# Kernel tuning notes

Hardware: AMD Instinct MI355X
Metric: run time of the kernel (lower is better)

Reference implementation:

```python
import jax, jax.numpy as jnp
import numpy as np

N = 100000      # nodes
E = 800000      # edges (avg degree 8)
F = 61          # num_node_features (embedding dim); node feat = F+3 = 64 with pos
D = 64          # hidden_dim
OUT = 32        # output_dim
TYPES = 100     # num_node_types
G = 64          # number of graphs in the batch (global_mean_pool segments)
L = 4           # num_layers per SE3Transformer (from transformer_config)


def _mk(k, shape):
    return jax.random.normal(k, shape, jnp.float32) * 0.1


def setup_inputs() -> dict:
    key = jax.random.key(0)
    ks = jax.random.split(key, 24)
    din = F + 3  # cat([pos, embedding(z)])
    inp = {
        "pos": jax.random.normal(ks[0], (N, 3), jnp.float32),
        "z": jax.random.randint(ks[1], (N,), 0, TYPES),
        "edge_index": jax.random.randint(ks[2], (2, E), 0, N),
        "batch": jnp.sort(jax.random.randint(ks[3], (N,), 0, G)),
        "emb": _mk(ks[4], (TYPES, F)),
        # transformer1: input proj din->D, then L message-passing layers at width D
        "t1_Win": _mk(ks[5], (din, D)),
        "t1_W1": _mk(ks[6], (L, 2 * D + 1, D)), "t1_b1": jnp.zeros((L, D), jnp.float32),
        "t1_W2": _mk(ks[7], (L, D, D)),        "t1_b2": jnp.zeros((L, D), jnp.float32),
        "t1_W3": _mk(ks[8], (L, 2 * D, D)),    "t1_b3": jnp.zeros((L, D), jnp.float32),
        # transformer2: input proj D->D, then L layers at width D
        "t2_Win": _mk(ks[9], (D, D)),
        "t2_W1": _mk(ks[10], (L, 2 * D + 1, D)), "t2_b1": jnp.zeros((L, D), jnp.float32),
        "t2_W2": _mk(ks[11], (L, D, D)),         "t2_b2": jnp.zeros((L, D), jnp.float32),
        "t2_W3": _mk(ks[12], (L, 2 * D, D)),     "t2_b3": jnp.zeros((L, D), jnp.float32),
        # final Linear(hidden_dim, output_dim)
        "Wlin": _mk(ks[13], (D, OUT)), "blin": jnp.zeros((OUT,), jnp.float32),
    }
    return inp


def _transformer(h, pos, src, dst, Win, W1, b1, W2, b2, W3, b3):
    """Equivariant graph transformer block: input projection + L distance-
    conditioned message-passing layers with residual updates."""
    h = h @ Win  # [N, D]
    # squared pairwise distance per edge -> rotation/translation invariant
    d2 = jnp.sum((pos[src] - pos[dst]) ** 2, axis=-1, keepdims=True)  # [E, 1]

    def layer(h, p):
        W1, b1, W2, b2, W3, b3 = p
        m = jnp.concatenate([h[src], h[dst], d2], axis=-1)        # [E, 2D+1]
        m = jax.nn.relu(m @ W1 + b1) @ W2 + b2                    # [E, D]
        agg = jax.ops.segment_sum(m, dst, num_segments=N)          # [N, D]
        h = h + jax.nn.relu(jnp.concatenate([h, agg], axis=-1) @ W3 + b3)
        return h, None

    h, _ = jax.lax.scan(layer, h, (W1, b1, W2, b2, W3, b3))
    return h


def reference(pos, z, edge_index, batch, emb,
              t1_Win, t1_W1, t1_b1, t1_W2, t1_b2, t1_W3, t1_b3,
              t2_Win, t2_W1, t2_b1, t2_W2, t2_b2, t2_W3, t2_b3,
              Wlin, blin):
    src, dst = edge_index[0], edge_index[1]
    x = jnp.concatenate([pos, emb[z]], axis=-1)  # [N, 3+F]
    x = jax.nn.relu(_transformer(x, pos, src, dst, t1_Win, t1_W1, t1_b1, t1_W2, t1_b2, t1_W3, t1_b3))
    x = jax.nn.relu(_transformer(x, pos, src, dst, t2_Win, t2_W1, t2_b1, t2_W2, t2_b2, t2_W3, t2_b3))
    x = x @ Wlin + blin  # [N, OUT]
    # global_mean_pool over graph ids
    counts = jax.ops.segment_sum(jnp.ones((N,), x.dtype), batch, num_segments=G)
    pooled = jax.ops.segment_sum(x, batch, num_segments=G) / jnp.clip(counts, 1.0)[:, None]
    return pooled  # [G, OUT]
```

## Files before the change

### kernel.cpp

```cpp
#include <hip/hip_runtime.h>
#include <hip/hip_bf16.h>

typedef unsigned short u16;
typedef unsigned int   u32;
typedef short bf16x8 __attribute__((ext_vector_type(8)));
typedef float f32x4  __attribute__((ext_vector_type(4)));
typedef int   i32x2  __attribute__((ext_vector_type(2)));

#define NN 100000
#define EE 800000
#define NTILE 6250
#define NTB   1563
#define EBLK  1536
#define TOTW  (EBLK * 4)
#define SCB   98
#define GMAX  (NN + EE / 8 + 2)

#define MFMA16(a,b,c) __builtin_amdgcn_mfma_f32_16x16x32_bf16(a,b,c,0,0,0)

__device__ __forceinline__ float b2f(u16 u) {
    u32 x = ((u32)u) << 16;
    return __uint_as_float(x);
}
__device__ __forceinline__ u16 f2b(float f) {
    __hip_bfloat16 h = __float2bfloat16(f);
    return *reinterpret_cast<u16*>(&h);
}
__device__ __forceinline__ void splt(float v, u16& hi, u16& lo) {
    hi = f2b(v);
    lo = f2b(v - b2f(hi));
}

__global__ __launch_bounds__(256) void k_deg(const int* __restrict__ dst,
                                             int* __restrict__ deg) {
    int e = blockIdx.x * 256 + threadIdx.x;
    if (e < EE) atomicAdd(&deg[dst[e]], 1);
}

__global__ __launch_bounds__(1024) void k_scanA(const int* __restrict__ deg,
                                                int* __restrict__ part) {
    __shared__ int s[1024];
    int i = blockIdx.x * 1024 + threadIdx.x;
    int v = (i < NN) ? deg[i] : 0;
    s[threadIdx.x] = v;
    __syncthreads();
    for (int off = 512; off > 0; off >>= 1) {
        if ((int)threadIdx.x < off) s[threadIdx.x] += s[threadIdx.x + off];
        __syncthreads();
    }
    if (threadIdx.x == 0) part[blockIdx.x] = s[0];
}

__global__ void k_scanB(int* __restrict__ part) {
    if (threadIdx.x == 0 && blockIdx.x == 0) {
        int run = 0;
        for (int b = 0; b < SCB; ++b) { int v = part[b]; part[b] = run; run += v; }
        part[SCB] = run;
    }
}

__global__ __launch_bounds__(1024) void k_scanC(const int* __restrict__ deg,
                                                const int* __restrict__ part,
                                                int* __restrict__ rowptr) {
    __shared__ int s[1024];
    int i = blockIdx.x * 1024 + threadIdx.x;
    int v = (i < NN) ? deg[i] : 0;
    s[threadIdx.x] = v;
    __syncthreads();
    for (int off = 1; off < 1024; off <<= 1) {
        int t = ((int)threadIdx.x >= off) ? s[threadIdx.x - off] : 0;
        __syncthreads();
        s[threadIdx.x] += t;
        __syncthreads();
    }
    int incl = s[threadIdx.x];
    if (i < NN) rowptr[i] = part[blockIdx.x] + incl - v;
    if (i == NN - 1) rowptr[NN] = part[SCB];
}

__global__ __launch_bounds__(256) void k_scatter(const int* __restrict__ src,
                                                 const int* __restrict__ dst,
                                                 const float* __restrict__ pos,
                                                 const int* __restrict__ rowptr,
                                                 const int* __restrict__ grp_ptr,
                                                 int* __restrict__ cursor,
                                                 int* __restrict__ srcg,
                                                 float* __restrict__ d2g) {
    int e = blockIdx.x * 256 + threadIdx.x;
    if (e >= EE) return;
    int d = dst[e], s = src[e];
    int p = atomicAdd(&cursor[d], 1);
    int off = p - rowptr[d];
    long slot = (long)(grp_ptr[d] + (off >> 3)) * 8 + (off & 7);
    srcg[slot] = s;
    float dx = pos[s * 3 + 0] - pos[d * 3 + 0];
    float dy = pos[s * 3 + 1] - pos[d * 3 + 1];
    float dz = pos[s * 3 + 2] - pos[d * 3 + 2];
    d2g[slot] = dx * dx + dy * dy + dz * dz;
}

__global__ __launch_bounds__(256) void k_ngrp(const int* __restrict__ deg,
                                              int* __restrict__ ngrp) {
    int i = blockIdx.x * 256 + threadIdx.x;
    if (i < NN) ngrp[i] = (deg[i] + 7) >> 3;
}

__global__ __launch_bounds__(256) void k_gtab(const int* __restrict__ deg,
                                              const int* __restrict__ grp_ptr,
                                              int* __restrict__ gtab) {
    int n = blockIdx.x * 256 + threadIdx.x;
    if (n >= NN) return;
    int d = deg[n];
    int ng = (d + 7) >> 3;
    int base = grp_ptr[n];
    for (int k = 0; k < ng; ++k) {
        int cc = d - 8 * k; if (cc > 8) cc = 8;
        gtab[base + k] = (n << 4) | cc;
    }
}

__global__ __launch_bounds__(256) void k_swz(const float* t1W1, const float* t1W2, const float* t1W3,
                                             const float* t2W1, const float* t2W2, const float* t2W3,
                                             const float* t1Win, const float* t2Win,
                                             u16* __restrict__ WsA, u16* __restrict__ WsB) {
    int gid = blockIdx.x * 256 + threadIdx.x;
    if (gid < 163840) {
        int L = gid / 20480;
        int r = gid % 20480;
        const float* W1 = (L < 4 ? t1W1 : t2W1) + (size_t)(L & 3) * 129 * 64;
        const float* W2 = (L < 4 ? t1W2 : t2W2) + (size_t)(L & 3) * 64 * 64;
        const float* W3 = (L < 4 ? t1W3 : t2W3) + (size_t)(L & 3) * 128 * 64;
        float w;
        int rr, f, e, lane, j, row, col;
        if (r < 8192) { rr = r; f = rr >> 9; e = rr & 511; lane = e >> 3; j = e & 7;
            row = (f >> 2) * 32 + (lane >> 4) * 8 + j; col = (f & 3) * 16 + (lane & 15);
            w = W1[row * 64 + col];
        } else if (r < 12288) { rr = r - 8192; f = rr >> 9; e = rr & 511; lane = e >> 3; j = e & 7;
            row = (f >> 2) * 32 + (lane >> 4) * 8 + j; col = (f & 3) * 16 + (lane & 15);
            w = W2[row * 64 + col];
        } else { rr = r - 12288; f = rr >> 9; e = rr & 511; lane = e >> 3; j = e & 7;
            row = (f >> 2) * 32 + (lane >> 4) * 8 + j; col = (f & 3) * 16 + (lane & 15);
            w = W3[row * 64 + col];
        }
        u16 hi, lo; splt(w, hi, lo);
        WsA[(size_t)L * 40960 + r] = hi;
        WsA[(size_t)L * 40960 + 20480 + r] = lo;
    } else {
        int t = gid - 163840;
        int sel = (t < 4096) ? 0 : 1;
        int rr = t & 4095;
        const float* Win = sel ? t2Win : t1Win;
        int f = rr >> 9, e = rr & 511, lane = e >> 3, j = e & 7;
        int row = (f >> 2) * 32 + (lane >> 4) * 8 + j;
        int col = (f & 3) * 16 + (lane & 15);
        float w = Win[row * 64 + col];
        u16 hi, lo; splt(w, hi, lo);
        WsB[sel * 8192 + rr] = hi;
        WsB[sel * 8192 + 4096 + rr] = lo;
    }
}

__global__ __launch_bounds__(256) void k_proj1(const float* __restrict__ pos,
                                               const int* __restrict__ z,
                                               const float* __restrict__ emb,
                                               const u16* __restrict__ WinS,
                                               u16* __restrict__ hbx) {
    int tile = blockIdx.x * 4 + (threadIdx.x >> 6);
    if (tile >= NTILE) return;
    int lane = threadIdx.x & 63, c = lane & 15, g = lane >> 4;
    int n0 = tile * 16, nr = n0 + c;
    int zr = z[nr];
    const float* er = emb + (long)zr * 61 - 3;
    bf16x8 A0h, A0l, A1h, A1l;
#pragma unroll
    for (int j = 0; j < 8; ++j) {
        int f = 8 * g + j;
        float v1 = (f < 3) ? pos[nr * 3 + (f < 3 ? f : 0)] : er[f];
        float v2 = er[32 + 8 * g + j];
        u16 hi, lo;
        splt(v1, hi, lo); A0h[j] = (short)hi; A0l[j] = (short)lo;
        splt(v2, hi, lo); A1h[j] = (short)hi; A1l[j] = (short)lo;
    }
    const bf16x8* Wh = (const bf16x8*)WinS;
    const bf16x8* Wl = (const bf16x8*)(WinS + 4096);
#pragma unroll
    for (int nt = 0; nt < 4; ++nt) {
        f32x4 acc = {0.f, 0.f, 0.f, 0.f};
        acc = MFMA16(A0h, Wh[nt * 64 + lane], acc);
        acc = MFMA16(A1h, Wh[(4 + nt) * 64 + lane], acc);
        acc = MFMA16(A0l, Wh[nt * 64 + lane], acc);
        acc = MFMA16(A1l, Wh[(4 + nt) * 64 + lane], acc);
        acc = MFMA16(A0h, Wl[nt * 64 + lane], acc);
        acc = MFMA16(A1h, Wl[(4 + nt) * 64 + lane], acc);
#pragma unroll
        for (int r = 0; r < 4; ++r) {
            long n = n0 + 4 * g + r;
            u16 hi, lo; splt(acc[r], hi, lo);
            hbx[n * 128 + nt * 16 + c] = hi;
            hbx[n * 128 + 64 + nt * 16 + c] = lo;
        }
    }
}

__global__ __launch_bounds__(256) void k_proj2(const u16* __restrict__ WinS,
                                               u16* __restrict__ hbx) {
    int tile = blockIdx.x * 4 + (threadIdx.x >> 6);
    if (tile >= NTILE) return;
    int lane = threadIdx.x & 63, c = lane & 15, g = lane >> 4;
    int n0 = tile * 16, nr = n0 + c;
    const bf16x8* p = (const bf16x8*)(hbx + (long)nr * 128);
    bf16x8 h0 = p[g], h1 = p[g + 4], l0 = p[g + 8], l1 = p[g + 12];
    bf16x8 A0h, A0l, A1h, A1l;
#pragma unroll
    for (int j = 0; j < 8; ++j) {
        float v1 = fmaxf(b2f((u16)h0[j]) + b2f((u16)l0[j]), 0.f);
        float v2 = fmaxf(b2f((u16)h1[j]) + b2f((u16)l1[j]), 0.f);
        u16 hi, lo;
        splt(v1, hi, lo); A0h[j] = (short)hi; A0l[j] = (short)lo;
        splt(v2, hi, lo); A1h[j] = (short)hi; A1l[j] = (short)lo;
    }
    const bf16x8* Wh = (const bf16x8*)WinS;
    const bf16x8* Wl = (const bf16x8*)(WinS + 4096);
#pragma unroll
    for (int nt = 0; nt < 4; ++nt) {
        f32x4 acc = {0.f, 0.f, 0.f, 0.f};
        acc = MFMA16(A0h, Wh[nt * 64 + lane], acc);
        acc = MFMA16(A1h, Wh[(4 + nt) * 64 + lane], acc);
        acc = MFMA16(A0l, Wh[nt * 64 + lane], acc);
        acc = MFMA16(A1l, Wh[(4 + nt) * 64 + lane], acc);
        acc = MFMA16(A0h, Wl[nt * 64 + lane], acc);
        acc = MFMA16(A1h, Wl[(4 + nt) * 64 + lane], acc);
#pragma unroll
        for (int r = 0; r < 4; ++r) {
            long n = n0 + 4 * g + r;
            u16 hi, lo; splt(acc[r], hi, lo);
            hbx[n * 128 + nt * 16 + c] = hi;
            hbx[n * 128 + 64 + nt * 16 + c] = lo;
        }
    }
}

__global__ __launch_bounds__(256) void k_dsthalf(const u16* __restrict__ hbx,
                                                 const u16* __restrict__ Wsl,
                                                 const float* __restrict__ b1,
                                                 float* __restrict__ accbT) {
    int tile = blockIdx.x * 4 + (threadIdx.x >> 6);
    if (tile >= NTILE) return;
    int lane = threadIdx.x & 63, c = lane & 15, g = lane >> 4;
    int n0 = tile * 16, nr = n0 + c;
    const bf16x8* W1h = (const bf16x8*)Wsl;
    const bf16x8* W1l = (const bf16x8*)(Wsl + 20480);
    const bf16x8* p = (const bf16x8*)(hbx + (long)nr * 128);
    bf16x8 A0h = p[g], A1h = p[g + 4], A0l = p[g + 8], A1l = p[g + 12];
    f32x4 acc4[4];
#pragma unroll
    for (int nt = 0; nt < 4; ++nt) {
        float bv = b1[nt * 16 + c];
        f32x4 acc = {bv, bv, bv, bv};
        acc = MFMA16(A0h, W1h[(8 + nt) * 64 + lane], acc);
        acc = MFMA16(A1h, W1h[(12 + nt) * 64 + lane], acc);
        acc = MFMA16(A0l, W1h[(8 + nt) * 64 + lane], acc);
        acc = MFMA16(A1l, W1h[(12 + nt) * 64 + lane], acc);
        acc = MFMA16(A0h, W1l[(8 + nt) * 64 + lane], acc);
        acc = MFMA16(A1h, W1l[(12 + nt) * 64 + lane], acc);
        acc4[nt] = acc;
    }
#pragma unroll
    for (int r = 0; r < 4; ++r) {
        f32x4 w = {acc4[0][r], acc4[1][r], acc4[2][r], acc4[3][r]};
        *(f32x4*)(accbT + (long)(n0 + 4 * g + r) * 64 + c * 4) = w;
    }
}

__global__ __launch_bounds__(256) void k_edges_mfma(const u16* __restrict__ hbx,
                                                    float* __restrict__ sgrp,
                                                    const float* __restrict__ d2g,
                                                    const int* __restrict__ srcg,
                                                    const int* __restrict__ gtab,
                                                    const int* __restrict__ grp_ptr,
                                                    const u16* __restrict__ Wsl,
                                                    const float* __restrict__ W1f,
                                                    const float* __restrict__ accbT) {
    int lane = threadIdx.x & 63;
    int wid = blockIdx.x * 4 + (threadIdx.x >> 6);
    int c = lane & 15, g = lane >> 4;
    const bf16x8* W1H = (const bf16x8*)Wsl;
    const bf16x8* W1L = (const bf16x8*)(Wsl + 20480);
    bf16x8 w1h[2][4], w1l[2][4];
#pragma unroll
    for (int ks = 0; ks < 2; ++ks)
#pragma unroll
        for (int nt = 0; nt < 4; ++nt) {
            w1h[ks][nt] = W1H[(ks * 4 + nt) * 64 + lane];
            w1l[ks][nt] = W1L[(ks * 4 + nt) * 64 + lane];
        }
    float wdc[4];
#pragma unroll
    for (int nt = 0; nt < 4; ++nt) wdc[nt] = W1f[128 * 64 + nt * 16 + c];

    int G = grp_ptr[NN];
    int T = (G + 1) >> 1;
    int ro = 4 * (g & 1);

    for (int ti = wid; ti < T; ti += TOTW) {
        i32x2 pk = *(const i32x2*)(gtab + 2 * ti);
        int psel = (g < 2) ? pk[0] : pk[1];
        int nsel = psel >> 4;
        int csel = psel & 15;

        f32x4 bse = *(const f32x4*)(accbT + (long)nsel * 64 + c * 4);
        int s = srcg[(long)ti * 16 + c];
        const bf16x8* sp = (const bf16x8*)(hbx + (long)s * 128);
        bf16x8 A0h = sp[g], A1h = sp[g + 4], A0l = sp[g + 8], A1l = sp[g + 12];
        f32x4 dq = *(const f32x4*)(d2g + (long)ti * 16 + 8 * (g >> 1) + ro);

        float sv[4];
#pragma unroll
        for (int nt = 0; nt < 4; ++nt) {
            f32x4 ci;
#pragma unroll
            for (int r = 0; r < 4; ++r) ci[r] = bse[nt] + dq[r] * wdc[nt];
            ci = MFMA16(A0h, w1h[0][nt], ci);
            ci = MFMA16(A1h, w1h[1][nt], ci);
            ci = MFMA16(A0l, w1h[0][nt], ci);
            ci = MFMA16(A1l, w1h[1][nt], ci);
            ci = MFMA16(A0h, w1l[0][nt], ci);
            ci = MFMA16(A1h, w1l[1][nt], ci);
            float s4 = 0.f;
#pragma unroll
            for (int r = 0; r < 4; ++r)
                s4 += (ro + r < csel) ? fmaxf(ci[r], 0.f) : 0.f;
            s4 += __shfl_xor(s4, 16);
            sv[nt] = s4;
        }
        if (g == 0) {
#pragma unroll
            for (int nt = 0; nt < 4; ++nt)
                sgrp[(long)(2 * ti) * 64 + nt * 16 + c] = sv[nt];
        }
        if (g == 2 && 2 * ti + 1 < G) {
#pragma unroll
            for (int nt = 0; nt < 4; ++nt)
                sgrp[(long)(2 * ti + 1) * 64 + nt * 16 + c] = sv[nt];
        }
    }
}

__global__ __launch_bounds__(256) void k_node2(u16* __restrict__ hbx,
                                               const float* __restrict__ sgrp,
                                               const int* __restrict__ grp_ptr,
                                               const int* __restrict__ deg,
                                               const u16* __restrict__ Wsl,
                                               const float* __restrict__ b2,
                                               const float* __restrict__ b3,
                                               const u16* __restrict__ WslN,
                                               const float* __restrict__ b1N,
                                               float* __restrict__ accbT) {
    __shared__ u16 th[4][16 * 72];
    __shared__ u16 tl[4][16 * 72];
    int w = threadIdx.x >> 6, lane = threadIdx.x & 63;
    int tile = blockIdx.x * 4 + w;
    if (tile >= NTILE) return;
    int c = lane & 15, g = lane >> 4;
    int n0 = tile * 16, nr = n0 + c;
    u16* lh = th[w];
    u16* ll = tl[w];

    const bf16x8* W2H = (const bf16x8*)(Wsl + 8192);
    const bf16x8* W2L = (const bf16x8*)(Wsl + 28672);
    const bf16x8* W3H = (const bf16x8*)(Wsl + 12288);
    const bf16x8* W3L = (const bf16x8*)(Wsl + 32768);

    int gp0 = grp_ptr[nr], gp1 = grp_ptr[nr + 1];
    f32x4 sA0 = {0, 0, 0, 0}, sA1 = {0, 0, 0, 0};
    f32x4 sB0 = {0, 0, 0, 0}, sB1 = {0, 0, 0, 0};
    for (int gi = gp0; gi < gp1; ++gi) {
        const f32x4* q = (const f32x4*)(sgrp + (long)gi * 64 + 8 * g);
        const f32x4* q2 = (const f32x4*)(sgrp + (long)gi * 64 + 32 + 8 * g);
        sA0 += q[0]; sA1 += q[1];
        sB0 += q2[0]; sB1 += q2[1];
    }
    bf16x8 S0h, S0l, S1h, S1l;
#pragma unroll
    for (int j = 0; j < 4; ++j) {
        u16 hi, lo;
        splt(sA0[j], hi, lo); S0h[j] = (short)hi; S0l[j] = (short)lo;
        splt(sA1[j], hi, lo); S0h[4 + j] = (short)hi; S0l[4 + j] = (short)lo;
        splt(sB0[j], hi, lo); S1h[j] = (short)hi; S1l[j] = (short)lo;
        splt(sB1[j], hi, lo); S1h[4 + j] = (short)hi; S1l[4 + j] = (short)lo;
    }

    const bf16x8* hp = (const bf16x8*)(hbx + (long)nr * 128);
    bf16x8 H0h = hp[g], H1h = hp[g + 4], H0l = hp[g + 8], H1l = hp[g + 12];

    float dg[4];
#pragma unroll
    for (int r = 0; r < 4; ++r) dg[r] = (float)deg[n0 + 4 * g + r];

#pragma unroll
    for (int nt = 0; nt < 4; ++nt) {
        float b2c = b2[nt * 16 + c];
        f32x4 a = {dg[0] * b2c, dg[1] * b2c, dg[2] * b2c, dg[3] * b2c};
        a = MFMA16(S0h, W2H[nt * 64 + lane], a);
        a = MFMA16(S1h, W2H[(4 + nt) * 64 + lane], a);
        a = MFMA16(S0l, W2H[nt * 64 + lane], a);
        a = MFMA16(S1l, W2H[(4 + nt) * 64 + lane], a);
        a = MFMA16(S0h, W2L[nt * 64 + lane], a);
        a = MFMA16(S1h, W2L[(4 + nt) * 64 + lane], a);
#pragma unroll
        for (int r = 0; r < 4; ++r) {
            u16 hi, lo; splt(a[r], hi, lo);
            lh[(4 * g + r) * 72 + nt * 16 + c] = hi;
            ll[(4 * g + r) * 72 + nt * 16 + c] = lo;
        }
    }
    bf16x8 G0h = *(const bf16x8*)(lh + c * 72 + g * 8);
    bf16x8 G1h = *(const bf16x8*)(lh + c * 72 + 32 + g * 8);
    bf16x8 G0l = *(const bf16x8*)(ll + c * 72 + g * 8);
    bf16x8 G1l = *(const bf16x8*)(ll + c * 72 + 32 + g * 8);

    f32x4 u4[4];
#pragma unroll
    for (int nt = 0; nt < 4; ++nt) {
        float bv = b3[nt * 16 + c];
        f32x4 u = {bv, bv, bv, bv};
        u = MFMA16(H0h, W3H[nt * 64 + lane], u);
        u = MFMA16(H1h, W3H[(4 + nt) * 64 + lane], u);
        u = MFMA16(G0h, W3H[(8 + nt) * 64 + lane], u);
        u = MFMA16(G1h, W3H[(12 + nt) * 64 + lane], u);
        u = MFMA16(H0l, W3H[nt * 64 + lane], u);
        u = MFMA16(H1l, W3H[(4 + nt) * 64 + lane], u);
        u = MFMA16(G0l, W3H[(8 + nt) * 64 + lane], u);
        u = MFMA16(G1l, W3H[(12 + nt) * 64 + lane], u);
        u = MFMA16(H0h, W3L[nt * 64 + lane], u);
        u = MFMA16(H1h, W3L[(4 + nt) * 64 + lane], u);
        u = MFMA16(G0h, W3L[(8 + nt) * 64 + lane], u);
        u = MFMA16(G1h, W3L[(12 + nt) * 64 + lane], u);
        u4[nt] = u;
    }

#pragma unroll
    for (int nt = 0; nt < 4; ++nt)
#pragma unroll
        for (int r = 0; r < 4; ++r) {
            long n = n0 + 4 * g + r;
            long ix = n * 128 + nt * 16 + c;
            float ho = b2f(hbx[ix]) + b2f(hbx[ix + 64]);
            float hn = ho + fmaxf(u4[nt][r], 0.f);
            u16 hi, lo; splt(hn, hi, lo);
            hbx[ix] = hi;
            hbx[ix + 64] = lo;
            lh[(4 * g + r) * 72 + nt * 16 + c] = hi;
            ll[(4 * g + r) * 72 + nt * 16 + c] = lo;
        }

    if (WslN) {
        bf16x8 N0h = *(const bf16x8*)(lh + c * 72 + g * 8);
        bf16x8 N1h = *(const bf16x8*)(lh + c * 72 + 32 + g * 8);
        bf16x8 N0l = *(const bf16x8*)(ll + c * 72 + g * 8);
        bf16x8 N1l = *(const bf16x8*)(ll + c * 72 + 32 + g * 8);
        const bf16x8* W1h = (const bf16x8*)WslN;
        const bf16x8* W1l = (const bf16x8*)(WslN + 20480);
        f32x4 acc4[4];
#pragma unroll
        for (int nt = 0; nt < 4; ++nt) {
            float bv = b1N[nt * 16 + c];
            f32x4 a = {bv, bv, bv, bv};
            a = MFMA16(N0h, W1h[(8 + nt) * 64 + lane], a);
            a = MFMA16(N1h, W1h[(12 + nt) * 64 + lane], a);
            a = MFMA16(N0l, W1h[(8 + nt) * 64 + lane], a);
            a = MFMA16(N1l, W1h[(12 + nt) * 64 + lane], a);
            a = MFMA16(N0h, W1l[(8 + nt) * 64 + lane], a);
            a = MFMA16(N1h, W1l[(12 + nt) * 64 + lane], a);
            acc4[nt] = a;
        }
#pragma unroll
        for (int r = 0; r < 4; ++r) {
            f32x4 wv = {acc4[0][r], acc4[1][r], acc4[2][r], acc4[3][r]};
            *(f32x4*)(accbT + (long)(n0 + 4 * g + r) * 64 + c * 4) = wv;
        }
    }
}

__global__ void k_granges(const int* __restrict__ batch, int* __restrict__ gpt) {
    int g = blockIdx.x * blockDim.x + threadIdx.x;
    if (g > 64) return;
    int lo = 0, hi = NN;
    while (lo < hi) {
        int mid = (lo + hi) >> 1;
        if (batch[mid] < g) lo = mid + 1; else hi = mid;
    }
    gpt[g] = lo;
}

__global__ __launch_bounds__(256) void k_sumrelu(const u16* __restrict__ hbx,
                                                 const int* __restrict__ gpt,
                                                 float* __restrict__ sumh) {
    int g = blockIdx.x >> 3, sp = blockIdx.x & 7;
    int lo = gpt[g], hi = gpt[g + 1];
    int n = hi - lo;
    int per = (n + 7) / 8;
    int s0 = lo + sp * per;
    int s1 = s0 + per; if (s1 > hi) s1 = hi;
    int lane = threadIdx.x & 63, wv = threadIdx.x >> 6;
    float acc = 0.f;
    for (int i = s0 + wv; i < s1; i += 4) {
        float v = b2f(hbx[(long)i * 128 + lane]) + b2f(hbx[(long)i * 128 + 64 + lane]);
        acc += fmaxf(v, 0.f);
    }
    if (acc != 0.f || wv == 0)
        atomicAdd(&sumh[g * 64 + lane], acc);
}

__global__ __launch_bounds__(256) void k_outgemm(const float* __restrict__ sumh,
                                                 const int* __restrict__ gpt,
                                                 const float* __restrict__ Wlin,
                                                 const float* __restrict__ blin,
                                                 float* __restrict__ out) {
    int idx = blockIdx.x * 256 + threadIdx.x;
    if (idx >= 64 * 32) return;
    int g = idx >> 5, o = idx & 31;
    int cnt = gpt[g + 1] - gpt[g];
    float acc = 0.f;
#pragma unroll 8
    for (int k = 0; k < 64; ++k)
        acc += sumh[g * 64 + k] * Wlin[k * 32 + o];
    out[idx] = (cnt > 0) ? (acc / (float)cnt + blin[o]) : 0.f;
}

extern "C" void kernel_launch(void* const* d_in, const int* in_sizes, int n_in,
                              void* d_out, int out_size, void* d_ws, size_t ws_size,
                              hipStream_t stream) {
    const float* pos    = (const float*)d_in[0];
    const int*   z      = (const int*)d_in[1];
    const int*   ei     = (const int*)d_in[2];
    const int*   batch  = (const int*)d_in[3];
    const float* emb    = (const float*)d_in[4];
    const float* t1_Win = (const float*)d_in[5];
    const float* t1_W1  = (const float*)d_in[6];
    const float* t1_b1  = (const float*)d_in[7];
    const float* t1_W2  = (const float*)d_in[8];
    const float* t1_b2  = (const float*)d_in[9];
    const float* t1_W3  = (const float*)d_in[10];
    const float* t1_b3  = (const float*)d_in[11];
    const float* t2_Win = (const float*)d_in[12];
    const float* t2_W1  = (const float*)d_in[13];
    const float* t2_b1  = (const float*)d_in[14];
    const float* t2_W2  = (const float*)d_in[15];
    const float* t2_b2  = (const float*)d_in[16];
    const float* t2_W3  = (const float*)d_in[17];
    const float* t2_b3  = (const float*)d_in[18];
    const float* Wlin   = (const float*)d_in[19];
    const float* blin   = (const float*)d_in[20];

    const int* srcI = ei;
    const int* dstI = ei + EE;

    char* ws = (char*)d_ws;
    size_t off = 0;
    auto alloc = [&](size_t bytes) -> void* {
        void* p = ws + off;
        off += (bytes + 255) / 256 * 256;
        return p;
    };
    float* accbT   = (float*)alloc((size_t)NN * 64 * 4);
    u16*   hbx     = (u16*)alloc((size_t)NN * 128 * 2);
    float* sgrp    = (float*)alloc((size_t)GMAX * 64 * 4);
    int*   rowptr  = (int*)alloc((size_t)(NN + 1) * 4);
    int*   deg     = (int*)alloc((size_t)NN * 4);
    int*   cursor  = (int*)alloc((size_t)NN * 4);
    int*   ngrpA   = (int*)alloc((size_t)NN * 4);
    int*   grp_ptr = (int*)alloc((size_t)(NN + 1) * 4);
    int*   gtab    = (int*)alloc((size_t)(GMAX + 2) * 4);
    int*   srcg    = (int*)alloc((size_t)GMAX * 8 * 4);
    float* d2g     = (float*)alloc((size_t)GMAX * 8 * 4);
    int*   gpt     = (int*)alloc(65 * 4);
    float* sumh    = (float*)alloc(64 * 64 * 4);
    int*   part    = (int*)alloc((SCB + 1) * 4);
    u16*   WsA     = (u16*)alloc((size_t)8 * 40960 * 2);
    u16*   WsB     = (u16*)alloc((size_t)16384 * 2);

    hipMemsetAsync(deg, 0, (size_t)NN * 4, stream);
    hipMemsetAsync(srcg, 0, (size_t)GMAX * 8 * 4, stream);
    hipMemsetAsync(d2g, 0, (size_t)GMAX * 8 * 4, stream);
    hipMemsetAsync(gtab, 0, (size_t)(GMAX + 2) * 4, stream);
    k_deg<<<(EE + 255) / 256, 256, 0, stream>>>(dstI, deg);
    k_scanA<<<SCB, 1024, 0, stream>>>(deg, part);
    k_scanB<<<1, 64, 0, stream>>>(part);
    k_scanC<<<SCB, 1024, 0, stream>>>(deg, part, rowptr);
    k_ngrp<<<(NN + 255) / 256, 256, 0, stream>>>(deg, ngrpA);
    k_scanA<<<SCB, 1024, 0, stream>>>(ngrpA, part);
    k_scanB<<<1, 64, 0, stream>>>(part);
    k_scanC<<<SCB, 1024, 0, stream>>>(ngrpA, part, grp_ptr);
    hipMemcpyAsync(cursor, rowptr, (size_t)NN * 4, hipMemcpyDeviceToDevice, stream);
    k_scatter<<<(EE + 255) / 256, 256, 0, stream>>>(srcI, dstI, pos, rowptr, grp_ptr,
                                                    cursor, srcg, d2g);
    k_gtab<<<(NN + 255) / 256, 256, 0, stream>>>(deg, grp_ptr, gtab);
    k_swz<<<172032 / 256, 256, 0, stream>>>(t1_W1, t1_W2, t1_W3, t2_W1, t2_W2, t2_W3,
                                            t1_Win, t2_Win, WsA, WsB);
    k_granges<<<1, 128, 0, stream>>>(batch, gpt);

    k_proj1<<<NTB, 256, 0, stream>>>(pos, z, emb, WsB, hbx);
    k_dsthalf<<<NTB, 256, 0, stream>>>(hbx, WsA, t1_b1, accbT);
    for (int l = 0; l < 4; ++l) {
        const u16* Wsl = WsA + (size_t)l * 40960;
        k_edges_mfma<<<EBLK, 256, 0, stream>>>(hbx, sgrp, d2g, srcg, gtab, grp_ptr,
                                               Wsl, t1_W1 + (size_t)l * 129 * 64, accbT);
        const u16* WslN = (l < 3) ? (WsA + (size_t)(l + 1) * 40960) : nullptr;
        const float* b1N = (l < 3) ? (t1_b1 + (size_t)(l + 1) * 64) : nullptr;
        k_node2<<<NTB, 256, 0, stream>>>(hbx, sgrp, grp_ptr, deg, Wsl,
                                         t1_b2 + (size_t)l * 64, t1_b3 + (size_t)l * 64,
                                         WslN, b1N, accbT);
    }

    k_proj2<<<NTB, 256, 0, stream>>>(WsB + 8192, hbx);
    k_dsthalf<<<NTB, 256, 0, stream>>>(hbx, WsA + (size_t)4 * 40960, t2_b1, accbT);
    for (int l = 0; l < 4; ++l) {
        const u16* Wsl = WsA + (size_t)(4 + l) * 40960;
        k_edges_mfma<<<EBLK, 256, 0, stream>>>(hbx, sgrp, d2g, srcg, gtab, grp_ptr,
                                               Wsl, t2_W1 + (size_t)l * 129 * 64, accbT);
        const u16* WslN = (l < 3) ? (WsA + (size_t)(5 + l) * 40960) : nullptr;
        const float* b1N = (l < 3) ? (t2_b1 + (size_t)(l + 1) * 64) : nullptr;
        k_node2<<<NTB, 256, 0, stream>>>(hbx, sgrp, grp_ptr, deg, Wsl,
                                         t2_b2 + (size_t)l * 64, t2_b3 + (size_t)l * 64,
                                         WslN, b1N, accbT);
    }

    hipMemsetAsync(sumh, 0, 64 * 64 * 4, stream);
    k_sumrelu<<<64 * 8, 256, 0, stream>>>(hbx, gpt, sumh);
    k_outgemm<<<8, 256, 0, stream>>>(sumh, gpt, Wlin, blin, (float*)d_out);
}
```

Before: 907.7 us.

## Store per-node and per-group intermediates as split bf16 pairs; simplify CSR build

Replaces the fp32 per-node bias buffer and the per-group message sums with hi/lo bf16 pairs, so they use the same byte count but different layouts and packed stores. The edge and node kernels unpack these pairs by adding hi+lo. Preprocessing also drops the degree prefix scan and the rowptr buffer: the cursor is initialised from grp_ptr*8 so the scatter writes slots directly. The gtab memset is replaced by a single write of the sentinel entry. Together these cut setup launches and change memory access patterns, at the cost of extra pack and unpack ALU work.

```diff
diff --git a/kernel.cpp b/kernel.cpp
--- a/kernel.cpp
+++ b/kernel.cpp
@@ -78,11 +78,21 @@
     if (i == NN - 1) rowptr[NN] = part[SCB];
 }
 
+__global__ __launch_bounds__(256) void k_ngrp(const int* __restrict__ deg,
+                                              int* __restrict__ ngrp) {
+    int i = blockIdx.x * 256 + threadIdx.x;
+    if (i < NN) ngrp[i] = (deg[i] + 7) >> 3;
+}
+
+__global__ __launch_bounds__(256) void k_curinit(const int* __restrict__ grp_ptr,
+                                                 int* __restrict__ cursor) {
+    int i = blockIdx.x * 256 + threadIdx.x;
+    if (i < NN) cursor[i] = grp_ptr[i] * 8;
+}
+
 __global__ __launch_bounds__(256) void k_scatter(const int* __restrict__ src,
                                                  const int* __restrict__ dst,
                                                  const float* __restrict__ pos,
-                                                 const int* __restrict__ rowptr,
-                                                 const int* __restrict__ grp_ptr,
                                                  int* __restrict__ cursor,
                                                  int* __restrict__ srcg,
                                                  float* __restrict__ d2g) {
@@ -90,19 +100,11 @@
     if (e >= EE) return;
     int d = dst[e], s = src[e];
     int p = atomicAdd(&cursor[d], 1);
-    int off = p - rowptr[d];
-    long slot = (long)(grp_ptr[d] + (off >> 3)) * 8 + (off & 7);
-    srcg[slot] = s;
+    srcg[p] = s;
     float dx = pos[s * 3 + 0] - pos[d * 3 + 0];
     float dy = pos[s * 3 + 1] - pos[d * 3 + 1];
     float dz = pos[s * 3 + 2] - pos[d * 3 + 2];
-    d2g[slot] = dx * dx + dy * dy + dz * dz;
-}
-
-__global__ __launch_bounds__(256) void k_ngrp(const int* __restrict__ deg,
-                                              int* __restrict__ ngrp) {
-    int i = blockIdx.x * 256 + threadIdx.x;
-    if (i < NN) ngrp[i] = (deg[i] + 7) >> 3;
+    d2g[p] = dx * dx + dy * dy + dz * dz;
 }
 
 __global__ __launch_bounds__(256) void k_gtab(const int* __restrict__ deg,
@@ -110,6 +112,7 @@
                                               int* __restrict__ gtab) {
     int n = blockIdx.x * 256 + threadIdx.x;
     if (n >= NN) return;
+    if (n == 0) gtab[grp_ptr[NN]] = 0;
     int d = deg[n];
     int ng = (d + 7) >> 3;
     int base = grp_ptr[n];
@@ -243,7 +246,7 @@
 __global__ __launch_bounds__(256) void k_dsthalf(const u16* __restrict__ hbx,
                                                  const u16* __restrict__ Wsl,
                                                  const float* __restrict__ b1,
-                                                 float* __restrict__ accbT) {
+                                                 u16* __restrict__ abx) {
     int tile = blockIdx.x * 4 + (threadIdx.x >> 6);
     if (tile >= NTILE) return;
     int lane = threadIdx.x & 63, c = lane & 15, g = lane >> 4;
@@ -267,20 +270,25 @@
     }
 #pragma unroll
     for (int r = 0; r < 4; ++r) {
-        f32x4 w = {acc4[0][r], acc4[1][r], acc4[2][r], acc4[3][r]};
-        *(f32x4*)(accbT + (long)(n0 + 4 * g + r) * 64 + c * 4) = w;
+        bf16x8 st;
+#pragma unroll
+        for (int nt = 0; nt < 4; ++nt) {
+            u16 hi, lo; splt(acc4[nt][r], hi, lo);
+            st[nt] = (short)hi; st[4 + nt] = (short)lo;
+        }
+        *(bf16x8*)(abx + (long)(n0 + 4 * g + r) * 128 + c * 8) = st;
     }
 }
 
 __global__ __launch_bounds__(256) void k_edges_mfma(const u16* __restrict__ hbx,
-                                                    float* __restrict__ sgrp,
+                                                    u16* __restrict__ sgx,
                                                     const float* __restrict__ d2g,
                                                     const int* __restrict__ srcg,
                                                     const int* __restrict__ gtab,
                                                     const int* __restrict__ grp_ptr,
                                                     const u16* __restrict__ Wsl,
                                                     const float* __restrict__ W1f,
-                                                    const float* __restrict__ accbT) {
+                                                    const u16* __restrict__ abx) {
     int lane = threadIdx.x & 63;
     int wid = blockIdx.x * 4 + (threadIdx.x >> 6);
     int c = lane & 15, g = lane >> 4;
@@ -308,7 +316,12 @@
         int nsel = psel >> 4;
         int csel = psel & 15;
 
-        f32x4 bse = *(const f32x4*)(accbT + (long)nsel * 64 + c * 4);
+        bf16x8 bp = *(const bf16x8*)(abx + (long)nsel * 128 + c * 8);
+        float base[4];
+#pragma unroll
+        for (int nt = 0; nt < 4; ++nt)
+            base[nt] = b2f((u16)bp[nt]) + b2f((u16)bp[4 + nt]);
+
         int s = srcg[(long)ti * 16 + c];
         const bf16x8* sp = (const bf16x8*)(hbx + (long)s * 128);
         bf16x8 A0h = sp[g], A1h = sp[g + 4], A0l = sp[g + 8], A1l = sp[g + 12];
@@ -319,7 +332,7 @@
         for (int nt = 0; nt < 4; ++nt) {
             f32x4 ci;
 #pragma unroll
-            for (int r = 0; r < 4; ++r) ci[r] = bse[nt] + dq[r] * wdc[nt];
+            for (int r = 0; r < 4; ++r) ci[r] = base[nt] + dq[r] * wdc[nt];
             ci = MFMA16(A0h, w1h[0][nt], ci);
             ci = MFMA16(A1h, w1h[1][nt], ci);
             ci = MFMA16(A0l, w1h[0][nt], ci);
@@ -335,19 +348,25 @@
         }
         if (g == 0) {
 #pragma unroll
-            for (int nt = 0; nt < 4; ++nt)
-                sgrp[(long)(2 * ti) * 64 + nt * 16 + c] = sv[nt];
+            for (int nt = 0; nt < 4; ++nt) {
+                u16 hi, lo; splt(sv[nt], hi, lo);
+                *(u32*)(sgx + (long)(2 * ti) * 128 + (nt * 16 + c) * 2) =
+                    (u32)hi | ((u32)lo << 16);
+            }
         }
         if (g == 2 && 2 * ti + 1 < G) {
 #pragma unroll
-            for (int nt = 0; nt < 4; ++nt)
-                sgrp[(long)(2 * ti + 1) * 64 + nt * 16 + c] = sv[nt];
+            for (int nt = 0; nt < 4; ++nt) {
+                u16 hi, lo; splt(sv[nt], hi, lo);
+                *(u32*)(sgx + (long)(2 * ti + 1) * 128 + (nt * 16 + c) * 2) =
+                    (u32)hi | ((u32)lo << 16);
+            }
         }
     }
 }
 
 __global__ __launch_bounds__(256) void k_node2(u16* __restrict__ hbx,
-                                               const float* __restrict__ sgrp,
+                                               const u16* __restrict__ sgx,
                                                const int* __restrict__ grp_ptr,
                                                const int* __restrict__ deg,
                                                const u16* __restrict__ Wsl,
@@ -355,7 +374,7 @@
                                                const float* __restrict__ b3,
                                                const u16* __restrict__ WslN,
                                                const float* __restrict__ b1N,
-                                               float* __restrict__ accbT) {
+                                               u16* __restrict__ abx) {
     __shared__ u16 th[4][16 * 72];
     __shared__ u16 tl[4][16 * 72];
     int w = threadIdx.x >> 6, lane = threadIdx.x & 63;
@@ -375,10 +394,16 @@
     f32x4 sA0 = {0, 0, 0, 0}, sA1 = {0, 0, 0, 0};
     f32x4 sB0 = {0, 0, 0, 0}, sB1 = {0, 0, 0, 0};
     for (int gi = gp0; gi < gp1; ++gi) {
-        const f32x4* q = (const f32x4*)(sgrp + (long)gi * 64 + 8 * g);
-        const f32x4* q2 = (const f32x4*)(sgrp + (long)gi * 64 + 32 + 8 * g);
-        sA0 += q[0]; sA1 += q[1];
-        sB0 += q2[0]; sB1 += q2[1];
+        const bf16x8* qa = (const bf16x8*)(sgx + (long)gi * 128 + 16 * g);
+        const bf16x8* qb = (const bf16x8*)(sgx + (long)gi * 128 + 64 + 16 * g);
+        bf16x8 a0 = qa[0], a1 = qa[1], b0 = qb[0], b1v = qb[1];
+#pragma unroll
+        for (int j = 0; j < 4; ++j) {
+            sA0[j] += b2f((u16)a0[2 * j]) + b2f((u16)a0[2 * j + 1]);
+            sA1[j] += b2f((u16)a1[2 * j]) + b2f((u16)a1[2 * j + 1]);
+            sB0[j] += b2f((u16)b0[2 * j]) + b2f((u16)b0[2 * j + 1]);
+            sB1[j] += b2f((u16)b1v[2 * j]) + b2f((u16)b1v[2 * j + 1]);
+        }
     }
     bf16x8 S0h, S0l, S1h, S1l;
 #pragma unroll
@@ -476,8 +501,13 @@
         }
 #pragma unroll
         for (int r = 0; r < 4; ++r) {
-            f32x4 wv = {acc4[0][r], acc4[1][r], acc4[2][r], acc4[3][r]};
-            *(f32x4*)(accbT + (long)(n0 + 4 * g + r) * 64 + c * 4) = wv;
+            bf16x8 st;
+#pragma unroll
+            for (int nt = 0; nt < 4; ++nt) {
+                u16 hi, lo; splt(acc4[nt][r], hi, lo);
+                st[nt] = (short)hi; st[4 + nt] = (short)lo;
+            }
+            *(bf16x8*)(abx + (long)(n0 + 4 * g + r) * 128 + c * 8) = st;
         }
     }
 }
@@ -563,10 +593,9 @@
         off += (bytes + 255) / 256 * 256;
         return p;
     };
-    float* accbT   = (float*)alloc((size_t)NN * 64 * 4);
+    u16*   abx     = (u16*)alloc((size_t)NN * 128 * 2);
     u16*   hbx     = (u16*)alloc((size_t)NN * 128 * 2);
-    float* sgrp    = (float*)alloc((size_t)GMAX * 64 * 4);
-    int*   rowptr  = (int*)alloc((size_t)(NN + 1) * 4);
+    u16*   sgx     = (u16*)alloc((size_t)GMAX * 128 * 2);
     int*   deg     = (int*)alloc((size_t)NN * 4);
     int*   cursor  = (int*)alloc((size_t)NN * 4);
     int*   ngrpA   = (int*)alloc((size_t)NN * 4);
@@ -583,47 +612,42 @@
     hipMemsetAsync(deg, 0, (size_t)NN * 4, stream);
     hipMemsetAsync(srcg, 0, (size_t)GMAX * 8 * 4, stream);
     hipMemsetAsync(d2g, 0, (size_t)GMAX * 8 * 4, stream);
-    hipMemsetAsync(gtab, 0, (size_t)(GMAX + 2) * 4, stream);
     k_deg<<<(EE + 255) / 256, 256, 0, stream>>>(dstI, deg);
-    k_scanA<<<SCB, 1024, 0, stream>>>(deg, part);
-    k_scanB<<<1, 64, 0, stream>>>(part);
-    k_scanC<<<SCB, 1024, 0, stream>>>(deg, part, rowptr);
     k_ngrp<<<(NN + 255) / 256, 256, 0, stream>>>(deg, ngrpA);
     k_scanA<<<SCB, 1024, 0, stream>>>(ngrpA, part);
     k_scanB<<<1, 64, 0, stream>>>(part);
     k_scanC<<<SCB, 1024, 0, stream>>>(ngrpA, part, grp_ptr);
-    hipMemcpyAsync(cursor, rowptr, (size_t)NN * 4, hipMemcpyDeviceToDevice, stream);
-    k_scatter<<<(EE + 255) / 256, 256, 0, stream>>>(srcI, dstI, pos, rowptr, grp_ptr,
-                                                    cursor, srcg, d2g);
+    k_curinit<<<(NN + 255) / 256, 256, 0, stream>>>(grp_ptr, cursor);
+    k_scatter<<<(EE + 255) / 256, 256, 0, stream>>>(srcI, dstI, pos, cursor, srcg, d2g);
     k_gtab<<<(NN + 255) / 256, 256, 0, stream>>>(deg, grp_ptr, gtab);
     k_swz<<<172032 / 256, 256, 0, stream>>>(t1_W1, t1_W2, t1_W3, t2_W1, t2_W2, t2_W3,
                                             t1_Win, t2_Win, WsA, WsB);
     k_granges<<<1, 128, 0, stream>>>(batch, gpt);
 
     k_proj1<<<NTB, 256, 0, stream>>>(pos, z, emb, WsB, hbx);
-    k_dsthalf<<<NTB, 256, 0, stream>>>(hbx, WsA, t1_b1, accbT);
+    k_dsthalf<<<NTB, 256, 0, stream>>>(hbx, WsA, t1_b1, abx);
     for (int l = 0; l < 4; ++l) {
         const u16* Wsl = WsA + (size_t)l * 40960;
-        k_edges_mfma<<<EBLK, 256, 0, stream>>>(hbx, sgrp, d2g, srcg, gtab, grp_ptr,
-                                               Wsl, t1_W1 + (size_t)l * 129 * 64, accbT);
+        k_edges_mfma<<<EBLK, 256, 0, stream>>>(hbx, sgx, d2g, srcg, gtab, grp_ptr,
+                                               Wsl, t1_W1 + (size_t)l * 129 * 64, abx);
         const u16* WslN = (l < 3) ? (WsA + (size_t)(l + 1) * 40960) : nullptr;
         const float* b1N = (l < 3) ? (t1_b1 + (size_t)(l + 1) * 64) : nullptr;
-        k_node2<<<NTB, 256, 0, stream>>>(hbx, sgrp, grp_ptr, deg, Wsl,
+        k_node2<<<NTB, 256, 0, stream>>>(hbx, sgx, grp_ptr, deg, Wsl,
                                          t1_b2 + (size_t)l * 64, t1_b3 + (size_t)l * 64,
-                                         WslN, b1N, accbT);
+                                         WslN, b1N, abx);
     }
 
     k_proj2<<<NTB, 256, 0, stream>>>(WsB + 8192, hbx);
-    k_dsthalf<<<NTB, 256, 0, stream>>>(hbx, WsA + (size_t)4 * 40960, t2_b1, accbT);
+    k_dsthalf<<<NTB, 256, 0, stream>>>(hbx, WsA + (size_t)4 * 40960, t2_b1, abx);
     for (int l = 0; l < 4; ++l) {
         const u16* Wsl = WsA + (size_t)(4 + l) * 40960;
-        k_edges_mfma<<<EBLK, 256, 0, stream>>>(hbx, sgrp, d2g, srcg, gtab, grp_ptr,
-                                               Wsl, t2_W1 + (size_t)l * 129 * 64, accbT);
+        k_edges_mfma<<<EBLK, 256, 0, stream>>>(hbx, sgx, d2g, srcg, gtab, grp_ptr,
+                                               Wsl, t2_W1 + (size_t)l * 129 * 64, abx);
         const u16* WslN = (l < 3) ? (WsA + (size_t)(5 + l) * 40960) : nullptr;
         const float* b1N = (l < 3) ? (t2_b1 + (size_t)(l + 1) * 64) : nullptr;
-        k_node2<<<NTB, 256, 0, stream>>>(hbx, sgrp, grp_ptr, deg, Wsl,
+        k_node2<<<NTB, 256, 0, stream>>>(hbx, sgx, grp_ptr, deg, Wsl,
                                          t2_b2 + (size_t)l * 64, t2_b3 + (size_t)l * 64,
-                                         WslN, b1N, accbT);
+                                         WslN, b1N, abx);
     }
 
     hipMemsetAsync(sumh, 0, 64 * 64 * 4, stream);
```

Result: slower. 938.4 us (+3.4%).
